# Kernel tuning notes

Measured on AMD Instinct MI355X. Metric: run time of the kernel, lower is better.

## Reference

```python
import jax, jax.numpy as jnp
import numpy as np

EPS = 1e-3  # batch_norm_epsilon


def _lstm_last(xs, W, U, b):
    """Keras-order LSTM (gates i,f,g,o); returns last hidden state [B,H]."""
    B = xs.shape[0]
    H = U.shape[0]

    def step(carry, xt):
        h, c = carry
        z = xt @ W + h @ U + b  # [B, 4H]
        i, f, g, o = jnp.split(z, 4, axis=-1)
        i = jax.nn.sigmoid(i)
        f = jax.nn.sigmoid(f)
        g = jnp.tanh(g)
        o = jax.nn.sigmoid(o)
        c = f * c + i * g
        h = o * jnp.tanh(c)
        return (h, c), None

    init = (jnp.zeros((B, H), xs.dtype), jnp.zeros((B, H), xs.dtype))
    (h, _), _ = jax.lax.scan(step, init, jnp.swapaxes(xs, 0, 1))
    return h


def setup_inputs() -> dict:
    key = jax.random.key(0)
    ks = jax.random.split(key, 10)
    B, T, C, H = 32, 512, 512, 512
    s_in = 1.0 / np.sqrt(C)
    s_rec = 1.0 / np.sqrt(H)
    return {
        "x": jax.random.normal(ks[0], (B, T, C), jnp.float32),
        # BatchNorm params (inference / moving stats)
        "gamma": jnp.ones((C,), jnp.float32),
        "beta": jnp.zeros((C,), jnp.float32),
        "moving_mean": jax.random.normal(ks[1], (C,), jnp.float32) * 0.1,
        "moving_var": jnp.abs(jax.random.normal(ks[2], (C,), jnp.float32)) * 0.1 + 1.0,
        # forward-direction LSTM
        "Wf": jax.random.normal(ks[3], (C, 4 * H), jnp.float32) * s_in,
        "Uf": jax.random.normal(ks[4], (H, 4 * H), jnp.float32) * s_rec,
        "bf": jnp.zeros((4 * H,), jnp.float32),
        # backward-direction LSTM
        "Wb": jax.random.normal(ks[5], (C, 4 * H), jnp.float32) * s_in,
        "Ub": jax.random.normal(ks[6], (H, 4 * H), jnp.float32) * s_rec,
        "bb": jnp.zeros((4 * H,), jnp.float32),
    }


def reference(x, gamma, beta, moving_mean, moving_var, Wf, Uf, bf, Wb, Ub, bb):
    # BatchNorm (inference) over last axis
    inv = jax.lax.rsqrt(moving_var + EPS)
    xn = (x - moving_mean) * inv * gamma + beta
    # Bidirectional LSTM, merge_mode='concat', return_sequences=False
    h_fwd = _lstm_last(xn, Wf, Uf, bf)
    h_bwd = _lstm_last(xn[:, ::-1, :], Wb, Ub, bb)
    return jnp.concatenate([h_fwd, h_bwd], axis=-1)  # [B, 2H]
```

## Files before the change

kernel.cpp:

```cpp
#include <hip/hip_runtime.h>
#include <stdint.h>

typedef __attribute__((ext_vector_type(8))) short short8;
typedef __attribute__((ext_vector_type(4))) float f32x4;
typedef __attribute__((ext_vector_type(2))) float f32x2;

#define NB 32
#define NT 512
#define NC 512
#define NH 512
#define NG 2048
#define WPD 32
#define NWG 64
#define UPW 16

__device__ __forceinline__ float bf2f(unsigned short u){
  union { unsigned int i; float f; } v; v.i = ((unsigned int)u) << 16; return v.f;
}
__device__ __forceinline__ unsigned short f2bf(float f){
  union { float f; unsigned int i; } v; v.f = f;
  unsigned int r = v.i + 0x7fffu + ((v.i >> 16) & 1u);
  return (unsigned short)(r >> 16);
}
__device__ __forceinline__ bool dt_fp32(const void* gamma){
  return ((const unsigned short*)gamma)[0] != 0x3F80;
}
__device__ __forceinline__ float ldv(const void* p, size_t i, bool f32){
  return f32 ? ((const float*)p)[i] : bf2f(((const unsigned short*)p)[i]);
}
__device__ __forceinline__ short8 frag_from_f32(const float* p){
  short8 r;
  #pragma unroll
  for (int j = 0; j < 8; ++j) r[j] = (short)f2bf(p[j]);
  return r;
}
__device__ __forceinline__ float sigm(float x){ return 1.f/(1.f + __expf(-x)); }
__device__ __forceinline__ float tanh_(float x){ return 1.f - 2.f/(1.f + __expf(2.f*x)); }

__device__ __forceinline__ unsigned int llc_load_u32(const unsigned int* p){
  unsigned int r;
  asm volatile("global_load_dword %0, %1, off sc0 sc1\n\ts_waitcnt vmcnt(0)"
               : "=v"(r) : "v"(p) : "memory");
  return r;
}
__device__ __forceinline__ void llc_store_u32(unsigned int* p, unsigned int v){
  asm volatile("global_store_dword %0, %1, off sc0 sc1" :: "v"(p), "v"(v) : "memory");
}
__device__ __forceinline__ void llc_load_hfrags(const unsigned short* p0,
                                                const unsigned short* p1,
                                                short8 hf[4][2]){
  asm volatile(
    "global_load_dwordx4 %0, %8, off sc0 sc1\n\t"
    "global_load_dwordx4 %1, %8, off offset:64 sc0 sc1\n\t"
    "global_load_dwordx4 %2, %8, off offset:128 sc0 sc1\n\t"
    "global_load_dwordx4 %3, %8, off offset:192 sc0 sc1\n\t"
    "global_load_dwordx4 %4, %9, off sc0 sc1\n\t"
    "global_load_dwordx4 %5, %9, off offset:64 sc0 sc1\n\t"
    "global_load_dwordx4 %6, %9, off offset:128 sc0 sc1\n\t"
    "global_load_dwordx4 %7, %9, off offset:192 sc0 sc1\n\t"
    "s_waitcnt vmcnt(0)"
    : "=&v"(hf[0][0]), "=&v"(hf[1][0]), "=&v"(hf[2][0]), "=&v"(hf[3][0]),
      "=&v"(hf[0][1]), "=&v"(hf[1][1]), "=&v"(hf[2][1]), "=&v"(hf[3][1])
    : "v"(p0), "v"(p1) : "memory");
}

__global__ void k_init(const void* __restrict__ gamma,
                       const void* __restrict__ beta,
                       const void* __restrict__ mmean,
                       const void* __restrict__ mvar,
                       float* __restrict__ scale, float* __restrict__ shift,
                       unsigned short* __restrict__ hbuf, unsigned int* __restrict__ flags){
  bool f32 = dt_fp32(gamma);
  int tid = blockIdx.x * 256 + threadIdx.x;
  if (blockIdx.x == 0){
    for (int c = threadIdx.x; c < NC; c += 256){
      float s = ldv(gamma, c, f32) * rsqrtf(ldv(mvar, c, f32) + 1e-3f);
      scale[c] = s;
      shift[c] = ldv(beta, c, f32) - ldv(mmean, c, f32) * s;
    }
    if (threadIdx.x < 64) flags[threadIdx.x] = 0u;
  }
  for (int i = tid; i < 2*2*NB*NH; i += gridDim.x * 256) hbuf[i] = 0;
}

__global__ void k_xcast(const void* __restrict__ x, const void* __restrict__ gamma,
                        unsigned short* __restrict__ x2){
  bool f32 = dt_fp32(gamma);
  int i = blockIdx.x * 256 + threadIdx.x;
  int c8 = i & 63;
  int rest = i >> 6;
  int t = rest & (NT - 1);
  int b = rest >> 9;
  size_t src = ((size_t)b * NT + t) * NC + c8 * 8;
  size_t dst = ((size_t)t * NB + b) * NC + c8 * 8;
  unsigned int pk[4];
  if (f32){
    const float* p = (const float*)x + src;
    #pragma unroll
    for (int j = 0; j < 4; ++j)
      pk[j] = (unsigned int)f2bf(p[2*j]) | ((unsigned int)f2bf(p[2*j+1]) << 16);
  } else {
    __builtin_memcpy(pk, (const unsigned short*)x + src, 16);
  }
  __builtin_memcpy(x2 + dst, pk, 16);
}

__global__ void k_bias(const void* __restrict__ Wf, const void* __restrict__ Wb,
                       const void* __restrict__ bfv, const void* __restrict__ bbv,
                       const void* __restrict__ gamma,
                       const float* __restrict__ shift, float* __restrict__ bias){
  bool f32 = dt_fp32(gamma);
  int id = blockIdx.x * 256 + threadIdx.x;
  int dir = id >> 11, n = id & 2047;
  const void* W = dir ? Wb : Wf;
  const void* b = dir ? bbv : bfv;
  float acc = ldv(b, n, f32);
  for (int c = 0; c < NC; ++c) acc += shift[c] * ldv(W, (size_t)c * NG + n, f32);
  bias[id] = acc;
}

__global__ __launch_bounds__(256, 1) void k_lstm(
    const void* __restrict__ x, const unsigned short* __restrict__ x2, int use_x2,
    const void* __restrict__ Wf, const void* __restrict__ Uf,
    const void* __restrict__ Wb, const void* __restrict__ Ub,
    const void* __restrict__ gamma,
    const float* __restrict__ scale, const float* __restrict__ bias,
    unsigned short* __restrict__ hbuf, unsigned int* __restrict__ flags,
    void* __restrict__ out){
  __shared__ float zbuf[4][NB][68];

  bool f32 = dt_fp32(gamma);
  int wg   = blockIdx.x;
  int dir  = wg & 1;
  int wgd  = wg >> 1;
  int ubase = wgd * UPW;
  const void* W = dir ? Wb : Wf;
  const void* U = dir ? Ub : Uf;
  int tid  = threadIdx.x;
  int lane = tid & 63, wave = tid >> 6;
  int m = lane & 15, q = lane >> 4;

  short8 bw[4][4], bu[4][4];
  #pragma unroll
  for (int kcl = 0; kcl < 4; ++kcl){
    int kc = wave * 4 + kcl;
    #pragma unroll
    for (int g = 0; g < 4; ++g){
      int col = g * NH + ubase + m;
      short8 vw, vu;
      #pragma unroll
      for (int j = 0; j < 8; ++j){
        int k = kc * 32 + q * 8 + j;
        vu[j] = (short)f2bf(ldv(U, (size_t)k * NG + col, f32));
        vw[j] = (short)f2bf(scale[k] * ldv(W, (size_t)k * NG + col, f32));
      }
      bw[kcl][g] = vw; bu[kcl][g] = vu;
    }
  }

  int pb = tid >> 3, pu2 = (tid & 7) * 2;
  float bias_r[2][4];
  #pragma unroll
  for (int g = 0; g < 4; ++g){
    bias_r[0][g] = bias[dir * NG + g * NH + ubase + pu2];
    bias_r[1][g] = bias[dir * NG + g * NH + ubase + pu2 + 1];
  }
  float cst[2] = {0.f, 0.f};

  unsigned int* myflags = flags + dir * 32;
  unsigned int* ownflag = myflags + wgd;
  unsigned short* hb0 = hbuf + (size_t)dir * 2 * NB * NH;

  short8 xf[4][2];
  {
    int tt0 = dir ? (NT - 1) : 0;
    #pragma unroll
    for (int kcl = 0; kcl < 4; ++kcl){
      int kc = wave * 4 + kcl;
      #pragma unroll
      for (int mt = 0; mt < 2; ++mt){
        if (use_x2){
          size_t xi = ((size_t)tt0 * NB + (mt * 16 + m)) * NC + kc * 32 + q * 8;
          __builtin_memcpy(&xf[kcl][mt], x2 + xi, 16);
        } else {
          size_t xi = ((size_t)(mt * 16 + m) * NT + tt0) * NC + kc * 32 + q * 8;
          if (f32) xf[kcl][mt] = frag_from_f32((const float*)x + xi);
          else     __builtin_memcpy(&xf[kcl][mt], (const unsigned short*)x + xi, 16);
        }
      }
    }
  }

  #pragma unroll 1
  for (int t = 0; t < NT; ++t){
    const unsigned short* hcur = hb0 + (size_t)(t & 1) * NB * NH;
    unsigned short* hnext = hb0 + (size_t)((t + 1) & 1) * NB * NH;

    f32x4 acc[4][2];
    #pragma unroll
    for (int g = 0; g < 4; ++g){
      acc[g][0] = (f32x4){0.f,0.f,0.f,0.f};
      acc[g][1] = (f32x4){0.f,0.f,0.f,0.f};
    }

    #pragma unroll
    for (int kcl = 0; kcl < 4; ++kcl)
      #pragma unroll
      for (int mt = 0; mt < 2; ++mt)
        #pragma unroll
        for (int g = 0; g < 4; ++g)
          acc[g][mt] = __builtin_amdgcn_mfma_f32_16x16x32_bf16(xf[kcl][mt], bw[kcl][g], acc[g][mt], 0, 0, 0);

    if (t < NT - 1){
      int ttn = dir ? (NT - 2 - t) : (t + 1);
      #pragma unroll
      for (int kcl = 0; kcl < 4; ++kcl){
        int kc = wave * 4 + kcl;
        #pragma unroll
        for (int mt = 0; mt < 2; ++mt){
          if (use_x2){
            size_t xi = ((size_t)ttn * NB + (mt * 16 + m)) * NC + kc * 32 + q * 8;
            __builtin_memcpy(&xf[kcl][mt], x2 + xi, 16);
          } else {
            size_t xi = ((size_t)(mt * 16 + m) * NT + ttn) * NC + kc * 32 + q * 8;
            if (f32) xf[kcl][mt] = frag_from_f32((const float*)x + xi);
            else     __builtin_memcpy(&xf[kcl][mt], (const unsigned short*)x + xi, 16);
          }
        }
      }
    }

    if (t > 0){
      unsigned int tgt = (unsigned int)t;
      while (true){
        unsigned int v = llc_load_u32(myflags + (lane & 31));
        if (__all((int)(v >= tgt))) break;
      }
    }

    short8 hf[4][2];
    llc_load_hfrags(hcur + (size_t)m * NH + wave * 128 + q * 8,
                    hcur + (size_t)(16 + m) * NH + wave * 128 + q * 8, hf);
    #pragma unroll
    for (int kcl = 0; kcl < 4; ++kcl)
      #pragma unroll
      for (int mt = 0; mt < 2; ++mt)
        #pragma unroll
        for (int g = 0; g < 4; ++g)
          acc[g][mt] = __builtin_amdgcn_mfma_f32_16x16x32_bf16(hf[kcl][mt], bu[kcl][g], acc[g][mt], 0, 0, 0);

    #pragma unroll
    for (int g = 0; g < 4; ++g)
      #pragma unroll
      for (int mt = 0; mt < 2; ++mt)
        #pragma unroll
        for (int r = 0; r < 4; ++r)
          zbuf[wave][mt * 16 + q * 4 + r][g * 16 + m] = acc[g][mt][r];
    __syncthreads();

    float z[2][4];
    #pragma unroll
    for (int g = 0; g < 4; ++g){ z[0][g] = bias_r[0][g]; z[1][g] = bias_r[1][g]; }
    #pragma unroll
    for (int w = 0; w < 4; ++w)
      #pragma unroll
      for (int g = 0; g < 4; ++g){
        f32x2 v = *(const f32x2*)&zbuf[w][pb][g * 16 + pu2];
        z[0][g] += v[0]; z[1][g] += v[1];
      }
    float hv[2];
    #pragma unroll
    for (int j = 0; j < 2; ++j){
      float iv = sigm(z[j][0]), fv = sigm(z[j][1]), gv = tanh_(z[j][2]), ov = sigm(z[j][3]);
      cst[j] = fv * cst[j] + iv * gv;
      hv[j] = ov * tanh_(cst[j]);
    }

    if (t == NT - 1){
      size_t o0 = (size_t)pb * (2 * NH) + dir * NH + ubase + pu2;
      if (f32){
        f32x2 ov2 = {hv[0], hv[1]};
        *(f32x2*)&((float*)out)[o0] = ov2;
      } else {
        unsigned int pk = (unsigned int)f2bf(hv[0]) | ((unsigned int)f2bf(hv[1]) << 16);
        *(unsigned int*)&((unsigned short*)out)[o0] = pk;
      }
      break;
    }

    {
      unsigned int pk = (unsigned int)f2bf(hv[0]) | ((unsigned int)f2bf(hv[1]) << 16);
      llc_store_u32((unsigned int*)(hnext + (size_t)pb * NH + ubase + pu2), pk);
    }

    __syncthreads();
    if (tid == 0) llc_store_u32(ownflag, (unsigned int)(t + 1));
  }
}

extern "C" void kernel_launch(void* const* d_in, const int* in_sizes, int n_in,
                              void* d_out, int out_size, void* d_ws, size_t ws_size,
                              hipStream_t stream){
  const void* x     = d_in[0];
  const void* gamma = d_in[1];
  const void* beta  = d_in[2];
  const void* mmean = d_in[3];
  const void* mvar  = d_in[4];
  const void* Wf    = d_in[5];
  const void* Uf    = d_in[6];
  const void* bfv   = d_in[7];
  const void* Wb    = d_in[8];
  const void* Ub    = d_in[9];
  const void* bbv   = d_in[10];

  char* ws = (char*)d_ws;
  float* scale = (float*)(ws + 0);
  float* shift = (float*)(ws + 2048);
  float* bias  = (float*)(ws + 4096);
  unsigned short* hbuf = (unsigned short*)(ws + 20480);
  unsigned int* flags  = (unsigned int*)(ws + 20480 + 131072);
  size_t x2_off = 20480 + 131072 + 4096;
  unsigned short* x2 = (unsigned short*)(ws + x2_off);
  size_t x2_bytes = (size_t)NT * NB * NC * 2;
  int use_x2 = (ws_size >= x2_off + x2_bytes) ? 1 : 0;

  hipLaunchKernelGGL(k_init, dim3(64),  dim3(256), 0, stream,
                     gamma, beta, mmean, mvar, scale, shift, hbuf, flags);
  if (use_x2)
    hipLaunchKernelGGL(k_xcast, dim3((NB*NT*NC/8)/256), dim3(256), 0, stream,
                       x, gamma, x2);
  hipLaunchKernelGGL(k_bias, dim3(16),  dim3(256), 0, stream,
                     Wf, Wb, bfv, bbv, gamma, shift, bias);
  hipLaunchKernelGGL(k_lstm, dim3(NWG), dim3(256), 0, stream,
                     x, x2, use_x2, Wf, Uf, Wb, Ub, gamma, scale, bias, hbuf, flags, d_out);
}
```

Before: 2.066 ms.

## Use per-wave step flags and ring buffers to drop end-of-step barrier

Each step now publishes one completion flag per wave instead of one per workgroup. Each wave polls only the 32 flags of the producer waves whose hidden-state slice it actually reads. The trailing __syncthreads is replaced by a per-wave vmcnt drain, so the h buffer grows to a 3-slot ring and the LDS gate buffer is double-buffered, letting waves run ahead safely. This trims workgroup-wide barrier latency on the serial recurrent critical path, at the cost of more flags, more LDS and more workspace.

```diff
diff --git a/kernel.cpp b/kernel.cpp
--- a/kernel.cpp
+++ b/kernel.cpp
@@ -13,6 +13,7 @@
 #define WPD 32
 #define NWG 64
 #define UPW 16
+#define NRING 3
 
 __device__ __forceinline__ float bf2f(unsigned short u){
   union { unsigned int i; float f; } v; v.i = ((unsigned int)u) << 16; return v.f;
@@ -45,6 +46,9 @@
 }
 __device__ __forceinline__ void llc_store_u32(unsigned int* p, unsigned int v){
   asm volatile("global_store_dword %0, %1, off sc0 sc1" :: "v"(p), "v"(v) : "memory");
+}
+__device__ __forceinline__ void vm_drain(){
+  asm volatile("s_waitcnt vmcnt(0)" ::: "memory");
 }
 __device__ __forceinline__ void llc_load_hfrags(const unsigned short* p0,
                                                 const unsigned short* p1,
@@ -78,9 +82,9 @@
       scale[c] = s;
       shift[c] = ldv(beta, c, f32) - ldv(mmean, c, f32) * s;
     }
-    if (threadIdx.x < 64) flags[threadIdx.x] = 0u;
-  }
-  for (int i = tid; i < 2*2*NB*NH; i += gridDim.x * 256) hbuf[i] = 0;
+    if (threadIdx.x < 2 * WPD * 4) flags[threadIdx.x] = 0u;
+  }
+  for (int i = tid; i < 2*NRING*NB*NH; i += gridDim.x * 256) hbuf[i] = 0;
 }
 
 __global__ void k_xcast(const void* __restrict__ x, const void* __restrict__ gamma,
@@ -127,7 +131,7 @@
     const float* __restrict__ scale, const float* __restrict__ bias,
     unsigned short* __restrict__ hbuf, unsigned int* __restrict__ flags,
     void* __restrict__ out){
-  __shared__ float zbuf[4][NB][68];
+  __shared__ float zbuf[2][4][NB][68];
 
   bool f32 = dt_fp32(gamma);
   int wg   = blockIdx.x;
@@ -167,9 +171,10 @@
   }
   float cst[2] = {0.f, 0.f};
 
-  unsigned int* myflags = flags + dir * 32;
-  unsigned int* ownflag = myflags + wgd;
-  unsigned short* hb0 = hbuf + (size_t)dir * 2 * NB * NH;
+  unsigned int* dflags = flags + dir * (WPD * 4);
+  unsigned int* ownflag = dflags + wgd * 4 + wave;
+  const unsigned int* pollp = dflags + 32 * wave + (lane & 31);
+  unsigned short* hb0 = hbuf + (size_t)dir * NRING * NB * NH;
 
   short8 xf[4][2];
   {
@@ -191,10 +196,13 @@
     }
   }
 
+  int par = 0;
+
   #pragma unroll 1
   for (int t = 0; t < NT; ++t){
-    const unsigned short* hcur = hb0 + (size_t)(t & 1) * NB * NH;
-    unsigned short* hnext = hb0 + (size_t)((t + 1) & 1) * NB * NH;
+    int parn = (par == NRING - 1) ? 0 : par + 1;
+    const unsigned short* hcur = hb0 + (size_t)par * NB * NH;
+    unsigned short* hnext = hb0 + (size_t)parn * NB * NH;
 
     f32x4 acc[4][2];
     #pragma unroll
@@ -233,7 +241,7 @@
     if (t > 0){
       unsigned int tgt = (unsigned int)t;
       while (true){
-        unsigned int v = llc_load_u32(myflags + (lane & 31));
+        unsigned int v = llc_load_u32(pollp);
         if (__all((int)(v >= tgt))) break;
       }
     }
@@ -249,23 +257,24 @@
         for (int g = 0; g < 4; ++g)
           acc[g][mt] = __builtin_amdgcn_mfma_f32_16x16x32_bf16(hf[kcl][mt], bu[kcl][g], acc[g][mt], 0, 0, 0);
 
+    int zp = t & 1;
     #pragma unroll
     for (int g = 0; g < 4; ++g)
       #pragma unroll
       for (int mt = 0; mt < 2; ++mt)
         #pragma unroll
         for (int r = 0; r < 4; ++r)
-          zbuf[wave][mt * 16 + q * 4 + r][g * 16 + m] = acc[g][mt][r];
+          zbuf[zp][wave][mt * 16 + q * 4 + r][g * 16 + m] = acc[g][mt][r];
     __syncthreads();
 
     float z[2][4];
     #pragma unroll
     for (int g = 0; g < 4; ++g){ z[0][g] = bias_r[0][g]; z[1][g] = bias_r[1][g]; }
     #pragma unroll
-    for (int w = 0; w < 4; ++w)
+    for (int wv = 0; wv < 4; ++wv)
       #pragma unroll
       for (int g = 0; g < 4; ++g){
-        f32x2 v = *(const f32x2*)&zbuf[w][pb][g * 16 + pu2];
+        f32x2 v = *(const f32x2*)&zbuf[zp][wv][pb][g * 16 + pu2];
         z[0][g] += v[0]; z[1][g] += v[1];
       }
     float hv[2];
@@ -292,9 +301,10 @@
       unsigned int pk = (unsigned int)f2bf(hv[0]) | ((unsigned int)f2bf(hv[1]) << 16);
       llc_store_u32((unsigned int*)(hnext + (size_t)pb * NH + ubase + pu2), pk);
     }
-
-    __syncthreads();
-    if (tid == 0) llc_store_u32(ownflag, (unsigned int)(t + 1));
+    vm_drain();
+    if (lane == 0) llc_store_u32(ownflag, (unsigned int)(t + 1));
+
+    par = parn;
   }
 }
 
@@ -318,8 +328,9 @@
   float* shift = (float*)(ws + 2048);
   float* bias  = (float*)(ws + 4096);
   unsigned short* hbuf = (unsigned short*)(ws + 20480);
-  unsigned int* flags  = (unsigned int*)(ws + 20480 + 131072);
-  size_t x2_off = 20480 + 131072 + 4096;
+  size_t flags_off = 20480 + (size_t)2 * NRING * NB * NH * 2;
+  unsigned int* flags  = (unsigned int*)(ws + flags_off);
+  size_t x2_off = (flags_off + 1024 + 255) & ~(size_t)255;
   unsigned short* x2 = (unsigned short*)(ws + x2_off);
   size_t x2_bytes = (size_t)NT * NB * NC * 2;
   int use_x2 = (ws_size >= x2_off + x2_bytes) ? 1 : 0;
```

After: 2.231 ms. 8.0% more time.
